# Performance work log

Measured on AMD Instinct MI355X. Metric: run time of the kernel, lower is better.

The kernel has to match this reference:

```python
import jax, jax.numpy as jnp
from jax import lax
import numpy as np

# ---- model dims ----
VOCAB, DMODEL, NLAYER = 32000, 1024, 4
NHEAD, HEAD = 16, 64              # RWKV6 heads (DMODEL = NHEAD*HEAD)
DIN = 2 * DMODEL                  # mamba expand=2
MHEAD, MHD = DIN // 64, 64        # mamba heads / head_dim (hard-coded 64 in block)
DSTATE, KCONV = 64, 4             # mamba2 state size / depthwise conv kernel
FFH = 4 * DMODEL
B, T = 1, 1024
EPS = 1e-6


def rmsnorm(v, w):
    return w * v * lax.rsqrt(jnp.mean(v * v, axis=-1, keepdims=True) + EPS)


def causal_dwconv(x, w):
    # x: [B,T,C], w: [C,K] depthwise causal conv
    C, K = w.shape
    xp = jnp.pad(x, ((0, 0), (K - 1, 0), (0, 0)))
    return lax.conv_general_dilated(
        xp, w.T[:, None, :], (1,), 'VALID',
        dimension_numbers=('NWC', 'WIO', 'NWC'), feature_group_count=C)


def setup_inputs() -> dict:
    key = jax.random.key(0)
    ks = iter(jax.random.split(key, 64))
    nrm = lambda shape, s=0.02: jax.random.normal(next(ks), shape, jnp.float32) * s
    x = jax.random.randint(next(ks), (B, T), 0, VOCAB)
    inp = dict(
        x=x,
        embed=nrm((VOCAB, DMODEL)),
        ln_w=jnp.ones((NLAYER, DMODEL), jnp.float32),
        Wr=nrm((NLAYER, DMODEL, DMODEL)), Wk=nrm((NLAYER, DMODEL, DMODEL)),
        Wv=nrm((NLAYER, DMODEL, DMODEL)), Ww=nrm((NLAYER, DMODEL, DMODEL)),
        w_bias=nrm((NLAYER, DMODEL), 0.5), u=nrm((NLAYER, NHEAD, HEAD), 0.5),
        Wg=nrm((NLAYER, DMODEL, DMODEL)), Wo=nrm((NLAYER, DMODEL, DMODEL)),
        Win=nrm((NLAYER, DMODEL, 2 * DIN + 2 * DSTATE + MHEAD)),
        conv_w=nrm((NLAYER, DIN + 2 * DSTATE, KCONV), 0.2),
        dt_bias=nrm((NLAYER, MHEAD), 0.5), A_log=nrm((NLAYER, MHEAD), 0.5),
        Dskip=nrm((NLAYER, MHEAD), 0.5),
        mnorm_w=jnp.ones((NLAYER, DIN), jnp.float32),
        Wout_m=nrm((NLAYER, DIN, DMODEL)),
        gate_w=nrm((NLAYER, 2 * DMODEL)), gate_b=jnp.zeros((NLAYER,), jnp.float32),
        ffn_ln_w=jnp.ones((NLAYER, DMODEL), jnp.float32),
        W1=nrm((NLAYER, DMODEL, FFH)), W2=nrm((NLAYER, FFH, DMODEL)),
        ln_out_w=jnp.ones((DMODEL,), jnp.float32),
    )
    return inp


def _block(h, p):
    (p_ln, pWr, pWk, pWv, pWw, p_wb, p_u, pWg, pWo, pWin, p_cw, p_dtb,
     p_Al, p_D, p_mn, pWom, p_gw, p_gb, p_fln, pW1, pW2) = p
    nx = rmsnorm(h, p_ln)

    # ---- RWKV6 linear attention ----
    r = (nx @ pWr).reshape(B, T, NHEAD, HEAD)
    k = (nx @ pWk).reshape(B, T, NHEAD, HEAD)
    v = (nx @ pWv).reshape(B, T, NHEAD, HEAD)
    dec = jnp.exp(-jnp.exp(nx @ pWw + p_wb)).reshape(B, T, NHEAD, HEAD)  # data-dep decay in (0,1)
    g = jax.nn.silu(nx @ pWg)

    def rstep(S, inp):
        rt, kt, vt, dt_ = inp                      # [B,H,hd]
        kv = kt[..., None] * vt[..., None, :]      # [B,H,hd,hd]
        o = jnp.einsum('bhk,bhkv->bhv', rt, S + p_u[None, :, :, None] * kv)
        return dt_[..., None] * S + kv, o

    S0 = jnp.zeros((B, NHEAD, HEAD, HEAD), nx.dtype)
    tmaj = lambda a: jnp.moveaxis(a, 1, 0)
    _, o = lax.scan(rstep, S0, (tmaj(r), tmaj(k), tmaj(v), tmaj(dec)))
    o = jnp.moveaxis(o, 0, 1).reshape(B, T, DMODEL)
    out_rwkv = (o * g) @ pWo

    # ---- Mamba2 selective scan ----
    zxbcdt = nx @ pWin
    z = zxbcdt[..., :DIN]
    xBC = zxbcdt[..., DIN:2 * DIN + 2 * DSTATE]
    dt = zxbcdt[..., -MHEAD:]
    xBC = jax.nn.silu(causal_dwconv(xBC, p_cw))
    xm = xBC[..., :DIN].reshape(B, T, MHEAD, MHD)
    Bm = xBC[..., DIN:DIN + DSTATE]
    Cm = xBC[..., DIN + DSTATE:]
    dt = jax.nn.softplus(dt + p_dtb)               # [B,T,MH]
    dA = jnp.exp(-dt * jnp.exp(p_Al))              # [B,T,MH]

    def mstep(hst, inp):
        xt, Bt, Ct, dAt, dtt = inp                 # [B,MH,hd],[B,ds],[B,ds],[B,MH],[B,MH]
        hst = dAt[..., None, None] * hst + (dtt[..., None] * xt)[..., None] * Bt[:, None, None, :]
        y = jnp.einsum('bhps,bs->bhp', hst, Ct)
        return hst, y

    h0 = jnp.zeros((B, MHEAD, MHD, DSTATE), nx.dtype)
    _, ym = lax.scan(mstep, h0, (tmaj(xm), tmaj(Bm), tmaj(Cm), tmaj(dA), tmaj(dt)))
    ym = jnp.moveaxis(ym, 0, 1) + p_D[None, None, :, None] * xm
    ym = ym.reshape(B, T, DIN)
    ym = rmsnorm(ym * jax.nn.silu(z), p_mn)        # gated RMSNorm
    out_mamba = ym @ pWom

    # ---- gated fusion + residual + FFN ----
    cat = jnp.concatenate([out_rwkv, out_mamba], axis=-1)
    gate = jax.nn.sigmoid(jnp.einsum('btd,d->bt', cat, p_gw) + p_gb)[..., None]
    h = h + gate * out_rwkv + (1.0 - gate) * out_mamba
    h = h + jax.nn.gelu(rmsnorm(h, p_fln) @ pW1, approximate=False) @ pW2
    return h


def reference(x, embed, ln_w, Wr, Wk, Wv, Ww, w_bias, u, Wg, Wo, Win, conv_w,
              dt_bias, A_log, Dskip, mnorm_w, Wout_m, gate_w, gate_b,
              ffn_ln_w, W1, W2, ln_out_w):
    h = embed[x]  # [B,T,D]
    params = (ln_w, Wr, Wk, Wv, Ww, w_bias, u, Wg, Wo, Win, conv_w, dt_bias,
              A_log, Dskip, mnorm_w, Wout_m, gate_w, gate_b, ffn_ln_w, W1, W2)
    h, _ = lax.scan(lambda c, p: (_block(c, p), None), h, params)
    logits = rmsnorm(h, ln_out_w) @ embed.T  # tied head
    return logits
```

## Files before the change

### kernel.cpp

```cpp
#include <hip/hip_runtime.h>
#include <hip/hip_bf16.h>
#include <math.h>

#define T 1024
#define NLAYER 4
#define NHEAD 16
#define HEAD 64
#define DIN 2048
#define MHEAD 32
#define DSTATE 64
#define FFH 4096
#define NWIN 4256
#define CCONV 2176
#define VOCABSZ 32000
#define NCHUNK 16
#define PKROWS 9472
#define PKN 9376

typedef unsigned short u16;
typedef __attribute__((ext_vector_type(8))) short s16x8;
typedef __attribute__((ext_vector_type(4))) float f32x4;

__device__ inline u16 f2bf(float f) {
  union { float f; unsigned u; } v; v.f = f;
  return (u16)((v.u + 0x7FFF + ((v.u >> 16) & 1)) >> 16);
}
__device__ inline float bf2f(u16 s) {
  union { unsigned u; float f; } v; v.u = ((unsigned)s) << 16;
  return v.f;
}
__device__ inline float sigf(float x) { return 1.f / (1.f + expf(-x)); }

__device__ inline void gload16(const void* g, void* l) {
  __builtin_amdgcn_global_load_lds(
      (__attribute__((address_space(1))) void*)(size_t)g,
      (__attribute__((address_space(3))) void*)(unsigned int)(size_t)l,
      16, 0, 0);
}

#define SWZ_SRC(lane) ((((lane) & 7) ^ ((lane) >> 3)) * 8)
#define SWZ_RD(kb, lk8, rsw) (((((kb) + (lk8)) >> 3) ^ (rsw)) << 3)

__device__ inline float block_sum(float v, float* sb) {
  #pragma unroll
  for (int o = 32; o; o >>= 1) v += __shfl_down(v, o);
  int w = threadIdx.x >> 6;
  if ((threadIdx.x & 63) == 0) sb[w] = v;
  __syncthreads();
  float s = sb[0] + sb[1] + sb[2] + sb[3];
  __syncthreads();
  return s;
}

__global__ __launch_bounds__(256) void k_cast(const float* __restrict__ s, u16* __restrict__ d) {
  size_t i = ((size_t)blockIdx.x * 256 + threadIdx.x) * 4;
  float4 v = *(const float4*)&s[i];
  u16 o[4] = {f2bf(v.x), f2bf(v.y), f2bf(v.z), f2bf(v.w)};
  *(uint2*)&d[i] = *(uint2*)o;
}

__global__ __launch_bounds__(256) void k_tcast(const float* __restrict__ src, size_t sstride,
                                               u16* __restrict__ dst, size_t dstride,
                                               int K, int N) {
  __shared__ float S[64][65];
  const float* sp = src + (size_t)blockIdx.z * sstride;
  u16* dp = dst + (size_t)blockIdx.z * dstride;
  int n0 = blockIdx.x * 64, k0 = blockIdx.y * 64;
  int tid = threadIdx.x;
  int tr = tid >> 4, tc = (tid & 15) * 4;
  #pragma unroll
  for (int it = 0; it < 4; ++it) {
    int r = tr + it * 16;
    int col = n0 + tc;
    float4 v;
    if (col + 3 < N) v = *(const float4*)&sp[(size_t)(k0 + r) * N + col];
    else {
      v.x = (col + 0 < N) ? sp[(size_t)(k0 + r) * N + col + 0] : 0.f;
      v.y = (col + 1 < N) ? sp[(size_t)(k0 + r) * N + col + 1] : 0.f;
      v.z = (col + 2 < N) ? sp[(size_t)(k0 + r) * N + col + 2] : 0.f;
      v.w = 0.f;
    }
    S[r][tc + 0] = v.x; S[r][tc + 1] = v.y; S[r][tc + 2] = v.z; S[r][tc + 3] = v.w;
  }
  __syncthreads();
  #pragma unroll
  for (int it = 0; it < 4; ++it) {
    int rn = tr + it * 16;
    if (n0 + rn >= N) continue;
    u16 o[4];
    o[0] = f2bf(S[tc + 0][rn]); o[1] = f2bf(S[tc + 1][rn]);
    o[2] = f2bf(S[tc + 2][rn]); o[3] = f2bf(S[tc + 3][rn]);
    *(uint2*)&dp[(size_t)(n0 + rn) * K + k0 + tc] = *(uint2*)o;
  }
}

struct TC6 { const float* src[6]; u16* dst[6]; size_t dstride[6]; };
__global__ __launch_bounds__(256) void k_tcast6(TC6 tc) {
  __shared__ float S[64][65];
  int w = blockIdx.z >> 2, l = blockIdx.z & 3;
  const float* sp = tc.src[w] + (size_t)l * 1024 * 1024;
  u16* dp = tc.dst[w] + (size_t)l * tc.dstride[w];
  int n0 = blockIdx.x * 64, k0 = blockIdx.y * 64;
  int tid = threadIdx.x;
  int tr = tid >> 4, tcc = (tid & 15) * 4;
  #pragma unroll
  for (int it = 0; it < 4; ++it) {
    int r = tr + it * 16;
    float4 v = *(const float4*)&sp[(size_t)(k0 + r) * 1024 + n0 + tcc];
    S[r][tcc + 0] = v.x; S[r][tcc + 1] = v.y; S[r][tcc + 2] = v.z; S[r][tcc + 3] = v.w;
  }
  __syncthreads();
  #pragma unroll
  for (int it = 0; it < 4; ++it) {
    int rn = tr + it * 16;
    u16 o[4];
    o[0] = f2bf(S[tcc + 0][rn]); o[1] = f2bf(S[tcc + 1][rn]);
    o[2] = f2bf(S[tcc + 2][rn]); o[3] = f2bf(S[tcc + 3][rn]);
    *(uint2*)&dp[(size_t)(n0 + rn) * 1024 + k0 + tcc] = *(uint2*)o;
  }
}

__global__ __launch_bounds__(256) void k_embln(const int* x, const float* embed,
                                               const float* w, float* h, u16* out) {
  __shared__ float sb[8];
  int t = blockIdx.x, tid = threadIdx.x;
  int row = x[t];
  float4 v = *(const float4*)&embed[(size_t)row * 1024 + tid * 4];
  *(float4*)&h[(size_t)t * 1024 + tid * 4] = v;
  float ss = v.x * v.x + v.y * v.y + v.z * v.z + v.w * v.w;
  float tot = block_sum(ss, sb);
  float rn = rsqrtf(tot / 1024.f + 1e-6f);
  int c = tid * 4;
  u16 o[4] = {f2bf(v.x * rn * w[c + 0]), f2bf(v.y * rn * w[c + 1]),
              f2bf(v.z * rn * w[c + 2]), f2bf(v.w * rn * w[c + 3])};
  *(uint2*)&out[(size_t)t * 1024 + c] = *(uint2*)o;
}

enum { EPI_F32 = 0, EPI_QKV = 1, EPI_GELU = 2 };

struct GOut {
  void* out;
  const float* aux;
  size_t zstride;
  float *r, *k, *v, *ld, *g, *zx;
};

template <int EPI, int BM, int BN>
__global__ __launch_bounds__(256) void k_gemm2(const u16* __restrict__ A,
                                               const u16* __restrict__ Bt,
                                               int N, int K, int kLen, GOut go) {
  __shared__ __align__(16) u16 smem[2][BM + BN][64];
  constexpr int FR = BM / 32, FC = BN / 32;
  constexpr int LPS = BM / 32 + BN / 32;
  int tid = threadIdx.x, lane = tid & 63, wid = tid >> 6;
  int lid = blockIdx.y * gridDim.x + blockIdx.x;
  int nwg = gridDim.x * gridDim.y;
  int q = nwg >> 3, r8 = nwg & 7;
  int xcd = lid & 7, pos = lid >> 3;
  int wg = (xcd < r8) ? (xcd * (q + 1) + pos) : (r8 * (q + 1) + (xcd - r8) * q + pos);
  int m0 = (wg % gridDim.x) * BM, n0 = (wg / gridDim.x) * BN;
  int kOff = blockIdx.z * kLen;
  int wr = (wid >> 1) * (BM / 2), wc = (wid & 1) * (BN / 2);
  int lr = lane & 15, lk8 = (lane >> 4) * 8;
  int rsw = lr & 7;
  int swc = SWZ_SRC(lane);
  int rA = lane >> 3;
  f32x4 acc[FR][FC] = {};

  auto STAGE = [&](int buf, int k0) {
    #pragma unroll
    for (int it = 0; it < BM / 32; ++it) {
      int rb = wid * (BM / 4) + it * 8;
      gload16(&A[(size_t)(m0 + rb + rA) * K + k0 + swc], &smem[buf][rb][0]);
    }
    #pragma unroll
    for (int it = 0; it < BN / 32; ++it) {
      int rb = wid * (BN / 4) + it * 8;
      gload16(&Bt[(size_t)(n0 + rb + rA) * K + k0 + swc], &smem[buf][BM + rb][0]);
    }
  };
  auto COMPUTE = [&](int buf) {
    #pragma unroll
    for (int kb = 0; kb < 64; kb += 32) {
      s16x8 af[FR], bf[FC];
      #pragma unroll
      for (int i = 0; i < FR; ++i)
        af[i] = *(const s16x8*)&smem[buf][wr + i * 16 + lr][SWZ_RD(kb, lk8, rsw)];
      #pragma unroll
      for (int j = 0; j < FC; ++j)
        bf[j] = *(const s16x8*)&smem[buf][BM + wc + j * 16 + lr][SWZ_RD(kb, lk8, rsw)];
      #pragma unroll
      for (int i = 0; i < FR; ++i)
        #pragma unroll
        for (int j = 0; j < FC; ++j)
          acc[i][j] = __builtin_amdgcn_mfma_f32_16x16x32_bf16(af[i], bf[j], acc[i][j], 0, 0, 0);
    }
  };

  int nt = kLen >> 6;
  STAGE(0, kOff);
  int cur = 0;
  for (int t = 0; t < nt; ++t) {
    if (t + 1 < nt) {
      STAGE(cur ^ 1, kOff + (t + 1) * 64);
      asm volatile("s_waitcnt vmcnt(%0)" :: "n"(LPS) : "memory");
    } else {
      asm volatile("s_waitcnt vmcnt(0)" ::: "memory");
    }
    __builtin_amdgcn_s_barrier();
    __builtin_amdgcn_sched_barrier(0);
    COMPUTE(cur);
    __builtin_amdgcn_s_barrier();
    cur ^= 1;
  }

  __syncthreads();
  float* cbuf = (float*)&smem[0][0][0];
  #pragma unroll
  for (int i = 0; i < FR; ++i)
    #pragma unroll
    for (int j = 0; j < FC; ++j) {
      int rrow = wr + i * 16 + ((lane >> 4) << 2);
      int ccol = wc + j * 16 + lr;
      #pragma unroll
      for (int r_ = 0; r_ < 4; ++r_)
        cbuf[(rrow + r_) * BN + ccol] = acc[i][j][r_];
    }
  __syncthreads();
  constexpr int RPB = BN / 4;
  constexpr int ITERS = (BM * RPB) / 256;
  if constexpr (EPI == EPI_F32) {
    float* outf = (float*)go.out + (size_t)blockIdx.z * go.zstride;
    #pragma unroll
    for (int it2 = 0; it2 < ITERS; ++it2) {
      int idx = it2 * 256 + tid;
      int row = idx / RPB, c4 = (idx % RPB) * 4;
      int gc = n0 + c4;
      if (gc >= N) continue;
      float4 v = *(const float4*)&cbuf[row * BN + c4];
      if (gc + 3 < N) *(float4*)&outf[(size_t)(m0 + row) * N + gc] = v;
      else {
        const float* pv = (const float*)&v;
        for (int e = 0; e < 4 && gc + e < N; ++e)
          outf[(size_t)(m0 + row) * N + gc + e] = pv[e];
      }
    }
  } else if constexpr (EPI == EPI_GELU) {
    u16* outb = (u16*)go.out;
    #pragma unroll
    for (int it2 = 0; it2 < ITERS; ++it2) {
      int idx = it2 * 256 + tid;
      int row = idx / RPB, c4 = (idx % RPB) * 4;
      int gc = n0 + c4;
      if (gc + 3 >= N) continue;
      float4 v = *(const float4*)&cbuf[row * BN + c4];
      u16 o[4];
      o[0] = f2bf(0.5f * v.x * (1.f + erff(v.x * 0.70710678118654752f)));
      o[1] = f2bf(0.5f * v.y * (1.f + erff(v.y * 0.70710678118654752f)));
      o[2] = f2bf(0.5f * v.z * (1.f + erff(v.z * 0.70710678118654752f)));
      o[3] = f2bf(0.5f * v.w * (1.f + erff(v.w * 0.70710678118654752f)));
      *(uint2*)&outb[(size_t)(m0 + row) * N + gc] = *(uint2*)o;
    }
  } else {
    float* tptr; int ldbw, coff, op;
    if (n0 < 5120) {
      int tsel = n0 >> 10;
      tptr = (tsel == 0) ? go.r : (tsel == 1) ? go.k : (tsel == 2) ? go.v
           : (tsel == 3) ? go.ld : go.g;
      ldbw = 1024; coff = n0 & 1023;
      op = (tsel == 3) ? 1 : (tsel == 4) ? 2 : 0;
    } else {
      tptr = go.zx; ldbw = 4256; coff = n0 - 5120; op = 0;
    }
    #pragma unroll
    for (int it2 = 0; it2 < ITERS; ++it2) {
      int idx = it2 * 256 + tid;
      int row = idx / RPB, c4 = (idx % RPB) * 4;
      int gc = n0 + c4;
      if (gc >= N) continue;
      float4 v = *(const float4*)&cbuf[row * BN + c4];
      float* pv = (float*)&v;
      if (op == 1) {
        #pragma unroll
        for (int e = 0; e < 4; ++e) pv[e] = -expf(pv[e] + go.aux[coff + c4 + e]);
      } else if (op == 2) {
        #pragma unroll
        for (int e = 0; e < 4; ++e) pv[e] = pv[e] * sigf(pv[e]);
      }
      if (gc + 3 < N) *(float4*)&tptr[(size_t)(m0 + row) * ldbw + coff + c4] = v;
      else {
        for (int e = 0; e < 4 && gc + e < N; ++e)
          tptr[(size_t)(m0 + row) * ldbw + coff + c4 + e] = pv[e];
      }
    }
  }
}

struct DualArg {
  const u16 *A0, *A1, *B0, *B1;
  float *o0, *o1;
  int K0, K1;
};
__global__ __launch_bounds__(256) void k_dual(DualArg da) {
  __shared__ __align__(16) u16 smem[2][128][64];
  const u16* A  = blockIdx.z ? da.A1 : da.A0;
  const u16* Bt = blockIdx.z ? da.B1 : da.B0;
  float* out    = blockIdx.z ? da.o1 : da.o0;
  int K         = blockIdx.z ? da.K1 : da.K0;
  const int N = 1024;
  int tid = threadIdx.x, lane = tid & 63, wid = tid >> 6;
  int lid = blockIdx.y * gridDim.x + blockIdx.x;
  int nwg = gridDim.x * gridDim.y;
  int q = nwg >> 3, r8 = nwg & 7;
  int xcd = lid & 7, pos = lid >> 3;
  int wg = (xcd < r8) ? (xcd * (q + 1) + pos) : (r8 * (q + 1) + (xcd - r8) * q + pos);
  int m0 = (wg % gridDim.x) * 64, n0 = (wg / gridDim.x) * 64;
  int wr = (wid >> 1) * 32, wc = (wid & 1) * 32;
  int lr = lane & 15, lk8 = (lane >> 4) * 8;
  int rsw = lr & 7, swc = SWZ_SRC(lane), rA = lane >> 3;
  f32x4 acc[2][2] = {};
  auto STAGE = [&](int buf, int k0) {
    #pragma unroll
    for (int it = 0; it < 2; ++it) {
      int rb = wid * 16 + it * 8;
      gload16(&A[(size_t)(m0 + rb + rA) * K + k0 + swc], &smem[buf][rb][0]);
      gload16(&Bt[(size_t)(n0 + rb + rA) * K + k0 + swc], &smem[buf][64 + rb][0]);
    }
  };
  auto COMPUTE = [&](int buf) {
    #pragma unroll
    for (int kb = 0; kb < 64; kb += 32) {
      s16x8 af[2], bf[2];
      #pragma unroll
      for (int i = 0; i < 2; ++i)
        af[i] = *(const s16x8*)&smem[buf][wr + i * 16 + lr][SWZ_RD(kb, lk8, rsw)];
      #pragma unroll
      for (int j = 0; j < 2; ++j)
        bf[j] = *(const s16x8*)&smem[buf][64 + wc + j * 16 + lr][SWZ_RD(kb, lk8, rsw)];
      #pragma unroll
      for (int i = 0; i < 2; ++i)
        #pragma unroll
        for (int j = 0; j < 2; ++j)
          acc[i][j] = __builtin_amdgcn_mfma_f32_16x16x32_bf16(af[i], bf[j], acc[i][j], 0, 0, 0);
    }
  };
  int nt = K >> 6;
  STAGE(0, 0);
  int cur = 0;
  for (int t = 0; t < nt; ++t) {
    if (t + 1 < nt) {
      STAGE(cur ^ 1, (t + 1) * 64);
      asm volatile("s_waitcnt vmcnt(4)" ::: "memory");
    } else {
      asm volatile("s_waitcnt vmcnt(0)" ::: "memory");
    }
    __builtin_amdgcn_s_barrier();
    __builtin_amdgcn_sched_barrier(0);
    COMPUTE(cur);
    __builtin_amdgcn_s_barrier();
    cur ^= 1;
  }
  __syncthreads();
  float* cbuf = (float*)&smem[0][0][0];
  #pragma unroll
  for (int i = 0; i < 2; ++i)
    #pragma unroll
    for (int j = 0; j < 2; ++j) {
      int rrow = wr + i * 16 + ((lane >> 4) << 2);
      int ccol = wc + j * 16 + lr;
      #pragma unroll
      for (int r_ = 0; r_ < 4; ++r_)
        cbuf[(rrow + r_) * 64 + ccol] = acc[i][j][r_];
    }
  __syncthreads();
  #pragma unroll
  for (int it2 = 0; it2 < 4; ++it2) {
    int idx = it2 * 256 + tid;
    int row = idx >> 4, c4 = (idx & 15) * 4;
    *(float4*)&out[(size_t)(m0 + row) * N + n0 + c4] = *(const float4*)&cbuf[row * 64 + c4];
  }
}

__global__ __launch_bounds__(256) void k_conv(const float* __restrict__ zx,
                                              const float* __restrict__ cw,
                                              float* __restrict__ xc) {
  int c = (blockIdx.x * 256 + threadIdx.x) * 4;
  int t = blockIdx.y;
  if (c >= CCONV) return;
  float4 w0 = *(const float4*)&cw[(c + 0) * 4];
  float4 w1 = *(const float4*)&cw[(c + 1) * 4];
  float4 w2 = *(const float4*)&cw[(c + 2) * 4];
  float4 w3 = *(const float4*)&cw[(c + 3) * 4];
  float4 a = {0.f, 0.f, 0.f, 0.f};
  #pragma unroll
  for (int tap = 0; tap < 4; ++tap) {
    int tt = t - 3 + tap;
    if (tt < 0) continue;
    float4 z = *(const float4*)&zx[(size_t)tt * NWIN + 2048 + c];
    a.x += z.x * ((const float*)&w0)[tap];
    a.y += z.y * ((const float*)&w1)[tap];
    a.z += z.z * ((const float*)&w2)[tap];
    a.w += z.w * ((const float*)&w3)[tap];
  }
  a.x = a.x * sigf(a.x); a.y = a.y * sigf(a.y);
  a.z = a.z * sigf(a.z); a.w = a.w * sigf(a.w);
  *(float4*)&xc[(size_t)t * CCONV + c] = a;
}

__global__ __launch_bounds__(256) void k_dtbc(const float* __restrict__ zx,
                                              const float* __restrict__ xc,
                                              const float* __restrict__ dt_bias,
                                              const float* __restrict__ A_log,
                                              float* __restrict__ dtb, float* __restrict__ la,
                                              float* __restrict__ BC) {
  int c = blockIdx.x, tid = threadIdx.x;
  if (blockIdx.y == 0) {
    __shared__ float ldaS[64][33];
    #pragma unroll
    for (int it = 0; it < 8; ++it) {
      int e = it * 256 + tid;
      int i = e >> 5, j = e & 31;
      float x = zx[(size_t)(c * 64 + i) * NWIN + 4224 + j] + dt_bias[j];
      float sp = (x > 20.f) ? x : log1pf(expf(x));
      dtb[(size_t)(c * 64 + i) * 32 + j] = sp;
      ldaS[i][j] = -sp * expf(A_log[j]);
    }
    __syncthreads();
    if (tid < 32) {
      float g = 0.f;
      for (int i = 0; i < 64; ++i) {
        g += ldaS[i][tid];
        la[((size_t)c * 32 + tid) * 64 + i] = g;
      }
    }
  } else {
    __shared__ float Bc[64][65];
    __shared__ float Cc[16][65];
    int i0 = (blockIdx.y - 1) * 16;
    #pragma unroll
    for (int it = 0; it < 4; ++it) {
      int idx = it * 256 + tid;
      int r = idx >> 4, c4 = (idx & 15) * 4;
      float4 b4 = *(const float4*)&xc[(size_t)(c * 64 + r) * CCONV + 2048 + c4];
      Bc[r][c4] = b4.x; Bc[r][c4+1] = b4.y; Bc[r][c4+2] = b4.z; Bc[r][c4+3] = b4.w;
    }
    {
      int r = tid >> 4, c4 = (tid & 15) * 4;
      float4 cv = *(const float4*)&xc[(size_t)(c * 64 + i0 + r) * CCONV + 2112 + c4];
      Cc[r][c4] = cv.x; Cc[r][c4+1] = cv.y; Cc[r][c4+2] = cv.z; Cc[r][c4+3] = cv.w;
    }
    __syncthreads();
    int il = tid >> 4, sg = tid & 15;
    float acc[4] = {};
    for (int d = 0; d < 64; ++d) {
      float cv = Cc[il][d];
      #pragma unroll
      for (int j = 0; j < 4; ++j) acc[j] += Bc[sg * 4 + j][d] * cv;
    }
    #pragma unroll
    for (int j = 0; j < 4; ++j)
      BC[((size_t)c * 64 + i0 + il) * 64 + sg * 4 + j] = acc[j];
  }
}

union SmemH1 {
  struct { float rS[64][66], kS[64][66], gS[64][66]; u16 khS[64][64]; u16 vtS[64][72]; float uS[64]; } a;
  struct { u16 XT[64][72], BT[64][72]; float fS[64]; } b;
};
__global__ __launch_bounds__(256) void k_heads1(const float* __restrict__ rbuf,
                                                const float* __restrict__ kbuf,
                                                const float* __restrict__ ldbuf,
                                                const float* __restrict__ vbuf,
                                                const float* __restrict__ u,
                                                const float* __restrict__ xc,
                                                const float* __restrict__ la,
                                                const float* __restrict__ dtb,
                                                u16* __restrict__ rt, float* __restrict__ eL,
                                                u16* __restrict__ G, float* __restrict__ U,
                                                float* __restrict__ Um) {
  __shared__ SmemH1 sm;
  int c = blockIdx.x, tid = threadIdx.x;
  int lane = tid & 63, wid = tid >> 6;
  int lr = lane & 15, lk8 = (lane >> 4) * 8, rsw = lr & 7;
  int wr = (wid >> 1) * 32, wc = (wid & 1) * 32;
  if (blockIdx.y < 16) {
    int h = blockIdx.y;
    #pragma unroll
    for (int it = 0; it < 4; ++it) {
      int idx = it * 256 + tid;
      int i = idx >> 4, c4 = (idx & 15) * 4;
      size_t base = (size_t)(c * 64 + i) * 1024 + h * 64 + c4;
      float4 rv = *(const float4*)&rbuf[base];
      float4 kv = *(const float4*)&kbuf[base];
      float4 lv = *(const float4*)&ldbuf[base];
      float4 vv = *(const float4*)&vbuf[base];
      sm.a.rS[i][c4] = rv.x; sm.a.rS[i][c4+1] = rv.y; sm.a.rS[i][c4+2] = rv.z; sm.a.rS[i][c4+3] = rv.w;
      sm.a.kS[i][c4] = kv.x; sm.a.kS[i][c4+1] = kv.y; sm.a.kS[i][c4+2] = kv.z; sm.a.kS[i][c4+3] = kv.w;
      sm.a.gS[i][c4] = lv.x; sm.a.gS[i][c4+1] = lv.y; sm.a.gS[i][c4+2] = lv.z; sm.a.gS[i][c4+3] = lv.w;
      sm.a.vtS[c4 + 0][i] = f2bf(vv.x); sm.a.vtS[c4 + 1][i] = f2bf(vv.y);
      sm.a.vtS[c4 + 2][i] = f2bf(vv.z); sm.a.vtS[c4 + 3][i] = f2bf(vv.w);
    }
    if (tid < 64) sm.a.uS[tid] = u[h * 64 + tid];
    __syncthreads();
    if (tid < 64) {
      int k = tid;
      float g = 0.f;
      for (int i = 0; i < 64; ++i) {
        float ld = sm.a.gS[i][k];
        sm.a.gS[i][k] = g;
        rt[(size_t)(c * 64 + i) * 1024 + h * 64 + k] = f2bf(sm.a.rS[i][k] * __expf(g));
        g += ld;
      }
      float gL = g;
      eL[((size_t)c * 16 + h) * 64 + k] = __expf(gL);
      for (int i = 0; i < 64; ++i) {
        float gincl = (i < 63) ? sm.a.gS[i + 1][k] : gL;
        int col = (((i >> 3) ^ (k & 7)) << 3) | (i & 7);
        sm.a.khS[k][col] = f2bf(sm.a.kS[i][k] * __expf(fminf(gL - gincl, 0.f)));
      }
    }
    __syncthreads();
    {
      int i = tid & 63, sg = tid >> 6;
      float acc[16] = {};
      float accd = 0.f;
      for (int k = 0; k < 64; ++k) {
        float rv = sm.a.rS[i][k], gi = sm.a.gS[i][k];
        accd += rv * sm.a.uS[k] * sm.a.kS[i][k];
        #pragma unroll
        for (int j = 0; j < 16; ++j) {
          int s = sg * 16 + j;
          int sp1 = (s < 63) ? s + 1 : 63;
          acc[j] += rv * sm.a.kS[s][k] * __expf(fminf(gi - sm.a.gS[sp1][k], 0.f));
        }
      }
      #pragma unroll
      for (int j = 0; j < 16; ++j) {
        int s = sg * 16 + j;
        float v = (s < i) ? acc[j] : ((s == i) ? accd : 0.f);
        G[(((size_t)c * 16 + h) * 64 + i) * 64 + s] = f2bf(v);
      }
    }
    {
      size_t gb = ((size_t)c * 16 + h) * 64;
      f32x4 acc2[2][2] = {};
      #pragma unroll
      for (int kb = 0; kb < 64; kb += 32) {
        s16x8 a[2], b[2];
        #pragma unroll
        for (int i_ = 0; i_ < 2; ++i_)
          a[i_] = *(const s16x8*)&sm.a.khS[wr + i_ * 16 + lr][SWZ_RD(kb, lk8, rsw)];
        #pragma unroll
        for (int j_ = 0; j_ < 2; ++j_)
          b[j_] = *(const s16x8*)&sm.a.vtS[wc + j_ * 16 + lr][kb + lk8];
        #pragma unroll
        for (int i_ = 0; i_ < 2; ++i_)
          #pragma unroll
          for (int j_ = 0; j_ < 2; ++j_)
            acc2[i_][j_] = __builtin_amdgcn_mfma_f32_16x16x32_bf16(a[i_], b[j_], acc2[i_][j_], 0, 0, 0);
      }
      #pragma unroll
      for (int i_ = 0; i_ < 2; ++i_)
        #pragma unroll
        for (int j_ = 0; j_ < 2; ++j_) {
          int row = wr + i_ * 16 + ((lane >> 4) << 2);
          int col = wc + j_ * 16 + lr;
          #pragma unroll
          for (int r_ = 0; r_ < 4; ++r_)
            U[(gb + row + r_) * 64 + col] = acc2[i_][j_][r_];
        }
    }
  } else {
    int h = blockIdx.y - 16;
    size_t lb = ((size_t)c * 32 + h) * 64;
    if (tid < 64) {
      float la63 = la[lb + 63];
      sm.b.fS[tid] = dtb[(size_t)(c * 64 + tid) * 32 + h] * __expf(fminf(la63 - la[lb + tid], 0.f));
    }
    __syncthreads();
    #pragma unroll
    for (int it = 0; it < 4; ++it) {
      int idx = it * 256 + tid;
      int t = idx >> 4, p4 = (idx & 15) * 4;
      float f = sm.b.fS[t];
      float4 xv = *(const float4*)&xc[(size_t)(c * 64 + t) * CCONV + h * 64 + p4];
      sm.b.XT[p4 + 0][t] = f2bf(f * xv.x); sm.b.XT[p4 + 1][t] = f2bf(f * xv.y);
      sm.b.XT[p4 + 2][t] = f2bf(f * xv.z); sm.b.XT[p4 + 3][t] = f2bf(f * xv.w);
      float4 bv = *(const float4*)&xc[(size_t)(c * 64 + t) * CCONV + 2048 + p4];
      sm.b.BT[p4 + 0][t] = f2bf(bv.x); sm.b.BT[p4 + 1][t] = f2bf(bv.y);
      sm.b.BT[p4 + 2][t] = f2bf(bv.z); sm.b.BT[p4 + 3][t] = f2bf(bv.w);
    }
    __syncthreads();
    f32x4 acc[2][2] = {};
    #pragma unroll
    for (int kb = 0; kb < 64; kb += 32) {
      s16x8 a[2], b[2];
      #pragma unroll
      for (int i = 0; i < 2; ++i) a[i] = *(const s16x8*)&sm.b.XT[wr + i * 16 + lr][kb + lk8];
      #pragma unroll
      for (int j = 0; j < 2; ++j) b[j] = *(const s16x8*)&sm.b.BT[wc + j * 16 + lr][kb + lk8];
      #pragma unroll
      for (int i = 0; i < 2; ++i)
        #pragma unroll
        for (int j = 0; j < 2; ++j)
          acc[i][j] = __builtin_amdgcn_mfma_f32_16x16x32_bf16(a[i], b[j], acc[i][j], 0, 0, 0);
    }
    #pragma unroll
    for (int i = 0; i < 2; ++i)
      #pragma unroll
      for (int j = 0; j < 2; ++j) {
        int row = wr + i * 16 + ((lane >> 4) << 2);
        int col = wc + j * 16 + lr;
        #pragma unroll
        for (int r_ = 0; r_ < 4; ++r_)
          Um[(lb + row + r_) * 64 + col] = acc[i][j][r_];
      }
  }
}

__global__ __launch_bounds__(256) void k_scan2(const float* __restrict__ Urw,
                                               const float* __restrict__ eL,
                                               u16* __restrict__ Sall,
                                               const float* __restrict__ Um,
                                               const float* __restrict__ la,
                                               u16* __restrict__ hall) {
  int tid = threadIdx.x;
  if (blockIdx.x < 16) {
    int h = blockIdx.x;
    int k = tid >> 2, v0 = blockIdx.y * 16 + (tid & 3) * 4;
    float S[4] = {};
    for (int c = 0; c < 16; ++c) {
      size_t gb = ((size_t)c * 16 + h) * 64;
      u16 tmp[4] = {f2bf(S[0]), f2bf(S[1]), f2bf(S[2]), f2bf(S[3])};
      *(uint2*)&Sall[(gb + k) * 64 + v0] = *(uint2*)&tmp[0];
      float e = eL[gb + k];
      float4 uv = *(const float4*)&Urw[(gb + k) * 64 + v0];
      S[0] = e * S[0] + uv.x; S[1] = e * S[1] + uv.y;
      S[2] = e * S[2] + uv.z; S[3] = e * S[3] + uv.w;
    }
  } else {
    int h = blockIdx.x - 16;
    int p = tid >> 2, s0 = blockIdx.y * 16 + (tid & 3) * 4;
    float S[4] = {};
    for (int c = 0; c < 16; ++c) {
      size_t lb = ((size_t)c * 32 + h) * 64;
      u16 tmp[4] = {f2bf(S[0]), f2bf(S[1]), f2bf(S[2]), f2bf(S[3])};
      *(uint2*)&hall[(lb + p) * 64 + s0] = *(uint2*)&tmp[0];
      float e = __expf(la[lb + 63]);
      float4 uv = *(const float4*)&Um[(lb + p) * 64 + s0];
      S[0] = e * S[0] + uv.x; S[1] = e * S[1] + uv.y;
      S[2] = e * S[2] + uv.z; S[3] = e * S[3] + uv.w;
    }
  }
}

union SmemH2 {
  struct { u16 rtS[64][64], GS[64][64], StS[64][72], vtS[64][72]; } a;
  struct { u16 MS[64][64], hS[64][64], CtS[64][72], XT2[64][72]; float laS[64], dtbS[64], eS[64]; } b;
};
__global__ __launch_bounds__(256) void k_heads2(const u16* __restrict__ rt,
                                                const u16* __restrict__ Gb,
                                                const u16* __restrict__ Sall,
                                                const float* __restrict__ vbuf,
                                                const float* __restrict__ gbuf,
                                                u16* __restrict__ og,
                                                const u16* __restrict__ hall,
                                                const float* __restrict__ xc,
                                                const float* __restrict__ la,
                                                const float* __restrict__ dtb,
                                                const float* __restrict__ BC,
                                                float* __restrict__ ymb) {
  __shared__ SmemH2 sm;
  int c = blockIdx.x, tid = threadIdx.x;
  int lane = tid & 63, wid = tid >> 6;
  int lr = lane & 15, lk8 = (lane >> 4) * 8;
  int rsw = lr & 7, swc = SWZ_SRC(lane);
  int wr = (wid >> 1) * 32, wc = (wid & 1) * 32;
  if (blockIdx.y < 16) {
    int h = blockIdx.y;
    size_t gb = ((size_t)c * 16 + h) * 64;
    #pragma unroll
    for (int it = 0; it < 2; ++it) {
      int rb = wid * 16 + it * 8;
      int r = rb + (lane >> 3);
      gload16(&rt[(size_t)(c * 64 + r) * 1024 + h * 64 + swc], &sm.a.rtS[rb][0]);
      gload16(&Gb[(gb + r) * 64 + swc], &sm.a.GS[rb][0]);
    }
    #pragma unroll
    for (int it = 0; it < 2; ++it) {
      int idx = it * 256 + tid;
      int k = idx >> 3, c8 = (idx & 7) * 8;
      uint4 ld = *(const uint4*)&Sall[(gb + k) * 64 + c8];
      const u16* pv = (const u16*)&ld;
      #pragma unroll
      for (int jj = 0; jj < 8; ++jj) sm.a.StS[c8 + jj][k] = pv[jj];
    }
    #pragma unroll
    for (int it = 0; it < 4; ++it) {
      int idx = it * 256 + tid;
      int s = idx >> 4, v4 = (idx & 15) * 4;
      float4 vv = *(const float4*)&vbuf[(size_t)(c * 64 + s) * 1024 + h * 64 + v4];
      sm.a.vtS[v4 + 0][s] = f2bf(vv.x); sm.a.vtS[v4 + 1][s] = f2bf(vv.y);
      sm.a.vtS[v4 + 2][s] = f2bf(vv.z); sm.a.vtS[v4 + 3][s] = f2bf(vv.w);
    }
    __syncthreads();
    f32x4 acc[2][2] = {};
    #pragma unroll
    for (int kb = 0; kb < 64; kb += 32) {
      s16x8 aR[2], aG[2], bS[2], bV[2];
      #pragma unroll
      for (int i = 0; i < 2; ++i) {
        aR[i] = *(const s16x8*)&sm.a.rtS[wr + i * 16 + lr][SWZ_RD(kb, lk8, rsw)];
        aG[i] = *(const s16x8*)&sm.a.GS[wr + i * 16 + lr][SWZ_RD(kb, lk8, rsw)];
      }
      #pragma unroll
      for (int j = 0; j < 2; ++j) {
        bS[j] = *(const s16x8*)&sm.a.StS[wc + j * 16 + lr][kb + lk8];
        bV[j] = *(const s16x8*)&sm.a.vtS[wc + j * 16 + lr][kb + lk8];
      }
      #pragma unroll
      for (int i = 0; i < 2; ++i)
        #pragma unroll
        for (int j = 0; j < 2; ++j) {
          acc[i][j] = __builtin_amdgcn_mfma_f32_16x16x32_bf16(aR[i], bS[j], acc[i][j], 0, 0, 0);
          acc[i][j] = __builtin_amdgcn_mfma_f32_16x16x32_bf16(aG[i], bV[j], acc[i][j], 0, 0, 0);
        }
    }
    #pragma unroll
    for (int i = 0; i < 2; ++i)
      #pragma unroll
      for (int j = 0; j < 2; ++j) {
        int row = c * 64 + wr + i * 16 + ((lane >> 4) << 2);
        int col = h * 64 + wc + j * 16 + lr;
        #pragma unroll
        for (int r_ = 0; r_ < 4; ++r_) {
          size_t idx = (size_t)(row + r_) * 1024 + col;
          og[idx] = f2bf(acc[i][j][r_] * gbuf[idx]);
        }
      }
  } else {
    int h = blockIdx.y - 16;
    size_t lb = ((size_t)c * 32 + h) * 64;
    if (tid < 64) {
      float lv = la[lb + tid];
      sm.b.laS[tid] = lv;
      sm.b.eS[tid] = __expf(lv);
      sm.b.dtbS[tid] = dtb[(size_t)(c * 64 + tid) * 32 + h];
    }
    #pragma unroll
    for (int it = 0; it < 2; ++it) {
      int rb = wid * 16 + it * 8;
      int r = rb + (lane >> 3);
      gload16(&hall[(lb + r) * 64 + swc], &sm.b.hS[rb][0]);
    }
    __syncthreads();
    #pragma unroll
    for (int it = 0; it < 4; ++it) {
      int idx = it * 256 + tid;
      int i = idx >> 4, s4 = (idx & 15) * 4;
      float lai = sm.b.laS[i];
      float4 bc4 = *(const float4*)&BC[((size_t)c * 64 + i) * 64 + s4];
      u16 mo[4];
      #pragma unroll
      for (int j = 0; j < 4; ++j) {
        int s = s4 + j;
        float bcv = (j == 0) ? bc4.x : (j == 1) ? bc4.y : (j == 2) ? bc4.z : bc4.w;
        float v = 0.f;
        if (s <= i)
          v = __expf(fminf(lai - sm.b.laS[s], 0.f)) * sm.b.dtbS[s] * bcv;
        mo[j] = f2bf(v);
      }
      *(uint2*)&sm.b.MS[i][(((s4 >> 3) ^ (i & 7)) << 3) | (s4 & 7)] = *(uint2*)mo;
      float ei = sm.b.eS[i];
      float4 cv = *(const float4*)&xc[(size_t)(c * 64 + i) * CCONV + 2112 + s4];
      sm.b.CtS[i][s4 + 0] = f2bf(ei * cv.x); sm.b.CtS[i][s4 + 1] = f2bf(ei * cv.y);
      sm.b.CtS[i][s4 + 2] = f2bf(ei * cv.z); sm.b.CtS[i][s4 + 3] = f2bf(ei * cv.w);
      float4 xv = *(const float4*)&xc[(size_t)(c * 64 + i) * CCONV + h * 64 + s4];
      sm.b.XT2[s4 + 0][i] = f2bf(xv.x); sm.b.XT2[s4 + 1][i] = f2bf(xv.y);
      sm.b.XT2[s4 + 2][i] = f2bf(xv.z); sm.b.XT2[s4 + 3][i] = f2bf(xv.w);
    }
    __syncthreads();
    f32x4 acc[2][2] = {};
    #pragma unroll
    for (int kb = 0; kb < 64; kb += 32) {
      s16x8 aM[2], aC[2], bX[2], bH[2];
      #pragma unroll
      for (int i = 0; i < 2; ++i) {
        aM[i] = *(const s16x8*)&sm.b.MS[wr + i * 16 + lr][SWZ_RD(kb, lk8, rsw)];
        aC[i] = *(const s16x8*)&sm.b.CtS[wr + i * 16 + lr][kb + lk8];
      }
      #pragma unroll
      for (int j = 0; j < 2; ++j) {
        bX[j] = *(const s16x8*)&sm.b.XT2[wc + j * 16 + lr][kb + lk8];
        bH[j] = *(const s16x8*)&sm.b.hS[wc + j * 16 + lr][SWZ_RD(kb, lk8, rsw)];
      }
      #pragma unroll
      for (int i = 0; i < 2; ++i)
        #pragma unroll
        for (int j = 0; j < 2; ++j) {
          acc[i][j] = __builtin_amdgcn_mfma_f32_16x16x32_bf16(aM[i], bX[j], acc[i][j], 0, 0, 0);
          acc[i][j] = __builtin_amdgcn_mfma_f32_16x16x32_bf16(aC[i], bH[j], acc[i][j], 0, 0, 0);
        }
    }
    #pragma unroll
    for (int i = 0; i < 2; ++i)
      #pragma unroll
      for (int j = 0; j < 2; ++j) {
        int row = c * 64 + wr + i * 16 + ((lane >> 4) << 2);
        int col = h * 64 + wc + j * 16 + lr;
        #pragma unroll
        for (int r_ = 0; r_ < 4; ++r_)
          ymb[(size_t)(row + r_) * 2048 + col] = acc[i][j][r_];
      }
  }
}

__global__ __launch_bounds__(256) void k_ymn(const float* ymb, const float* xc,
                                             const float* zx, const float* Dsk,
                                             const float* mnw, u16* out) {
  __shared__ float sb[8];
  int t = blockIdx.x, tid = threadIdx.x;
  float vals[8];
  float ss = 0.f;
  #pragma unroll
  for (int j = 0; j < 8; ++j) {
    int cidx = j * 256 + tid;
    float yv = ymb[(size_t)t * 2048 + cidx] + Dsk[cidx >> 6] * xc[(size_t)t * CCONV + cidx];
    float zv = zx[(size_t)t * NWIN + cidx];
    float val = yv * zv * sigf(zv);
    vals[j] = val;
    ss += val * val;
  }
  float tot = block_sum(ss, sb);
  float rn = rsqrtf(tot / 2048.f + 1e-6f);
  #pragma unroll
  for (int j = 0; j < 8; ++j) {
    int cidx = j * 256 + tid;
    out[(size_t)t * 2048 + cidx] = f2bf(vals[j] * rn * mnw[cidx]);
  }
}

__global__ __launch_bounds__(256) void k_gateln(const float* rw, const float* mb,
                                                const float* gw, const float* gb,
                                                float* h, const float* w, u16* nx) {
  __shared__ float sb[8];
  int t = blockIdx.x, tid = threadIdx.x;
  float s = 0.f;
  #pragma unroll
  for (int j = 0; j < 4; ++j) {
    int d = j * 256 + tid;
    s += rw[(size_t)t * 1024 + d] * gw[d] + mb[(size_t)t * 1024 + d] * gw[1024 + d];
  }
  float tot = block_sum(s, sb);
  float gate = sigf(tot + gb[0]);
  float hv[4], ss = 0.f;
  #pragma unroll
  for (int j = 0; j < 4; ++j) {
    int d = j * 256 + tid;
    float v = h[(size_t)t * 1024 + d] + gate * rw[(size_t)t * 1024 + d] +
              (1.f - gate) * mb[(size_t)t * 1024 + d];
    h[(size_t)t * 1024 + d] = v;
    hv[j] = v;
    ss += v * v;
  }
  float tot2 = block_sum(ss, sb);
  float rn = rsqrtf(tot2 / 1024.f + 1e-6f);
  #pragma unroll
  for (int j = 0; j < 4; ++j) {
    int d = j * 256 + tid;
    nx[(size_t)t * 1024 + d] = f2bf(hv[j] * rn * w[d]);
  }
}

__global__ __launch_bounds__(256) void k_redln(const float* __restrict__ part,
                                               float* __restrict__ h,
                                               const float* __restrict__ w,
                                               u16* __restrict__ nx) {
  __shared__ float sb[8];
  int t = blockIdx.x, tid = threadIdx.x;
  size_t base = (size_t)t * 1024 + tid * 4;
  float4 s = *(const float4*)&part[base];
  #pragma unroll
  for (int p = 1; p < 4; ++p) {
    float4 v = *(const float4*)&part[(size_t)p * 1024 * 1024 + base];
    s.x += v.x; s.y += v.y; s.z += v.z; s.w += v.w;
  }
  float4 d = *(const float4*)&h[base];
  s.x += d.x; s.y += d.y; s.z += d.z; s.w += d.w;
  *(float4*)&h[base] = s;
  float ss = s.x * s.x + s.y * s.y + s.z * s.z + s.w * s.w;
  float tot = block_sum(ss, sb);
  float rn = rsqrtf(tot / 1024.f + 1e-6f);
  int c = tid * 4;
  u16 o[4] = {f2bf(s.x * rn * w[c + 0]), f2bf(s.y * rn * w[c + 1]),
              f2bf(s.z * rn * w[c + 2]), f2bf(s.w * rn * w[c + 3])};
  *(uint2*)&nx[(size_t)t * 1024 + c] = *(uint2*)o;
}

extern "C" void kernel_launch(void* const* d_in, const int* in_sizes, int n_in,
                              void* d_out, int out_size, void* d_ws, size_t ws_size,
                              hipStream_t stream) {
  const int*   x       = (const int*)d_in[0];
  const float* embed   = (const float*)d_in[1];
  const float* ln_w    = (const float*)d_in[2];
  const float* Wr      = (const float*)d_in[3];
  const float* Wk      = (const float*)d_in[4];
  const float* Wv      = (const float*)d_in[5];
  const float* Ww      = (const float*)d_in[6];
  const float* w_bias  = (const float*)d_in[7];
  const float* u       = (const float*)d_in[8];
  const float* Wg      = (const float*)d_in[9];
  const float* Wo      = (const float*)d_in[10];
  const float* Win     = (const float*)d_in[11];
  const float* conv_w  = (const float*)d_in[12];
  const float* dt_bias = (const float*)d_in[13];
  const float* A_log   = (const float*)d_in[14];
  const float* Dskip   = (const float*)d_in[15];
  const float* mnorm_w = (const float*)d_in[16];
  const float* Wout_m  = (const float*)d_in[17];
  const float* gate_w  = (const float*)d_in[18];
  const float* gate_b  = (const float*)d_in[19];
  const float* ffn_ln  = (const float*)d_in[20];
  const float* W1      = (const float*)d_in[21];
  const float* W2      = (const float*)d_in[22];
  const float* ln_out  = (const float*)d_in[23];

  char* p = (char*)d_ws;
  auto alloc = [&](size_t bytes) {
    char* r = p;
    p += (bytes + 255) & ~(size_t)255;
    return r;
  };
  u16* embB = (u16*)alloc((size_t)VOCABSZ * 1024 * 2);
  u16* Wpk  = (u16*)alloc((size_t)NLAYER * PKROWS * 1024 * 2);
  u16* WoT  = (u16*)alloc((size_t)NLAYER * 1024 * 1024 * 2);
  u16* WomT = (u16*)alloc((size_t)NLAYER * 1024 * 2048 * 2);
  u16* W1T  = (u16*)alloc((size_t)NLAYER * 4096 * 1024 * 2);
  u16* W2T  = (u16*)alloc((size_t)NLAYER * 1024 * 4096 * 2);
  float* h        = (float*)alloc((size_t)T * 1024 * 4);
  u16*   nx       = (u16*)alloc((size_t)T * 1024 * 2);
  float* rbuf     = (float*)alloc((size_t)T * 1024 * 4);
  float* kbuf     = (float*)alloc((size_t)T * 1024 * 4);
  float* vbuf     = (float*)alloc((size_t)T * 1024 * 4);
  float* ldbuf    = (float*)alloc((size_t)T * 1024 * 4);
  float* gbuf     = (float*)alloc((size_t)T * 1024 * 4);
  float* zx       = (float*)alloc((size_t)T * NWIN * 4);
  u16*   rt       = (u16*)alloc((size_t)T * 1024 * 2);
  float* eL       = (float*)alloc((size_t)NCHUNK * 16 * 64 * 4);
  u16*   Gb       = (u16*)alloc((size_t)NCHUNK * 16 * 64 * 64 * 2);
  float* Urw      = (float*)alloc((size_t)NCHUNK * 16 * 64 * 64 * 4);
  u16*   Sall     = (u16*)alloc((size_t)NCHUNK * 16 * 64 * 64 * 2);
  u16*   og       = (u16*)alloc((size_t)T * 1024 * 2);
  float* out_rwkv = (float*)alloc((size_t)T * 1024 * 4);
  float* xc       = (float*)alloc((size_t)T * CCONV * 4);
  float* dtb      = (float*)alloc((size_t)T * 32 * 4);
  float* la       = (float*)alloc((size_t)NCHUNK * 32 * 64 * 4);
  float* BC       = (float*)alloc((size_t)NCHUNK * 64 * 64 * 4);
  float* Um       = (float*)alloc((size_t)NCHUNK * 32 * 64 * 64 * 4);
  u16*   hall     = (u16*)alloc((size_t)NCHUNK * 32 * 64 * 64 * 2);
  float* ymb      = (float*)alloc((size_t)T * 2048 * 4);
  u16*   ymn      = (u16*)alloc((size_t)T * 2048 * 2);
  float* out_mam  = (float*)alloc((size_t)T * 1024 * 4);
  u16*   ffa      = (u16*)alloc((size_t)T * FFH * 2);
  float* part     = (float*)alloc((size_t)4 * 1024 * 1024 * 4);

  const size_t PKS = (size_t)PKROWS * 1024;

  k_cast<<<VOCABSZ * 1024 / 1024, 256, 0, stream>>>(embed, embB);
  {
    TC6 tc;
    tc.src[0] = Wr; tc.src[1] = Wk; tc.src[2] = Wv; tc.src[3] = Ww; tc.src[4] = Wg; tc.src[5] = Wo;
    tc.dst[0] = Wpk;               tc.dstride[0] = PKS;
    tc.dst[1] = Wpk + 1024 * 1024; tc.dstride[1] = PKS;
    tc.dst[2] = Wpk + 2048 * 1024; tc.dstride[2] = PKS;
    tc.dst[3] = Wpk + 3072 * 1024; tc.dstride[3] = PKS;
    tc.dst[4] = Wpk + 4096 * 1024; tc.dstride[4] = PKS;
    tc.dst[5] = WoT;               tc.dstride[5] = (size_t)1024 * 1024;
    k_tcast6<<<dim3(16, 16, 24), 256, 0, stream>>>(tc);
  }
  k_tcast<<<dim3(67, 16, 4), 256, 0, stream>>>(Win, (size_t)1024 * NWIN, Wpk + (size_t)5120 * 1024, PKS, 1024, NWIN);
  k_tcast<<<dim3(16, 32, 4), 256, 0, stream>>>(Wout_m, (size_t)2048 * 1024, WomT, (size_t)1024 * 2048, 2048, 1024);
  k_tcast<<<dim3(64, 16, 4), 256, 0, stream>>>(W1, (size_t)1024 * 4096, W1T, (size_t)4096 * 1024, 1024, 4096);
  k_tcast<<<dim3(16, 64, 4), 256, 0, stream>>>(W2, (size_t)4096 * 1024, W2T, (size_t)1024 * 4096, 4096, 1024);

  k_embln<<<1024, 256, 0, stream>>>(x, embed, ln_w, h, nx);

  for (int l = 0; l < NLAYER; ++l) {
    {
      GOut go = {};
      go.r = rbuf; go.k = kbuf; go.v = vbuf; go.ld = ldbuf; go.g = gbuf; go.zx = zx;
      go.aux = w_bias + l * 1024;
      k_gemm2<EPI_QKV, 128, 128><<<dim3(8, 74), 256, 0, stream>>>(nx, Wpk + (size_t)l * PKS, PKN, 1024, 1024, go);
    }
    k_conv<<<dim3(3, 1024), 256, 0, stream>>>(zx, conv_w + (size_t)l * CCONV * 4, xc);
    k_dtbc<<<dim3(16, 5), 256, 0, stream>>>(zx, xc, dt_bias + l * 32, A_log + l * 32, dtb, la, BC);
    k_heads1<<<dim3(16, 48), 256, 0, stream>>>(rbuf, kbuf, ldbuf, vbuf, u + (size_t)l * 1024,
                                               xc, la, dtb, rt, eL, Gb, Urw, Um);
    k_scan2<<<dim3(48, 4), 256, 0, stream>>>(Urw, eL, Sall, Um, la, hall);
    k_heads2<<<dim3(16, 48), 256, 0, stream>>>(rt, Gb, Sall, vbuf, gbuf, og,
                                               hall, xc, la, dtb, BC, ymb);
    k_ymn<<<1024, 256, 0, stream>>>(ymb, xc, zx, Dskip + l * 32, mnorm_w + (size_t)l * 2048, ymn);
    {
      DualArg da;
      da.A0 = og;  da.B0 = WoT + (size_t)l * 1024 * 1024;  da.o0 = out_rwkv; da.K0 = 1024;
      da.A1 = ymn; da.B1 = WomT + (size_t)l * 1024 * 2048; da.o1 = out_mam;  da.K1 = 2048;
      k_dual<<<dim3(16, 16, 2), 256, 0, stream>>>(da);
    }
    k_gateln<<<1024, 256, 0, stream>>>(out_rwkv, out_mam, gate_w + (size_t)l * 2048,
                                       gate_b + l, h, ffn_ln + l * 1024, nx);
    {
      GOut go = {}; go.out = ffa;
      k_gemm2<EPI_GELU, 128, 128><<<dim3(8, 32), 256, 0, stream>>>(nx, W1T + (size_t)l * 4096 * 1024, 4096, 1024, 1024, go);
    }
    {
      GOut go = {}; go.out = part; go.zstride = (size_t)1024 * 1024;
      k_gemm2<EPI_F32, 64, 64><<<dim3(16, 16, 4), 256, 0, stream>>>(ffa, W2T + (size_t)l * 1024 * 4096, 1024, 4096, 1024, go);
    }
    k_redln<<<1024, 256, 0, stream>>>(part, h,
                                      (l < NLAYER - 1) ? (ln_w + (l + 1) * 1024) : ln_out, nx);
  }

  {
    GOut go = {}; go.out = d_out;
    k_gemm2<EPI_F32, 128, 128><<<dim3(8, 250), 256, 0, stream>>>(nx, embB, VOCABSZ, 1024, 1024, go);
  }
}
```

Baseline: 1.106 ms.

## Generalize GEMM to 512-thread blocks and store F32 outputs directly from registers

The GEMM kernel is templated on thread count, so 128x128 tiles now run with 8 waves in a 4x2 layout instead of 4 waves, which halves the accumulator fragments per wave and adds latency hiding. Staging loads are unified across the A and B rows. The F32 epilogue now writes accumulators straight to global memory, dropping the LDS round-trip and two barriers, but the stores become scalar and strided per lane instead of float4 rows. The larger blocks may also lower how many workgroups fit per CU.

```diff
diff --git a/kernel.cpp b/kernel.cpp
--- a/kernel.cpp
+++ b/kernel.cpp
@@ -145,13 +145,18 @@
   float *r, *k, *v, *ld, *g, *zx;
 };
 
-template <int EPI, int BM, int BN>
-__global__ __launch_bounds__(256) void k_gemm2(const u16* __restrict__ A,
-                                               const u16* __restrict__ Bt,
-                                               int N, int K, int kLen, GOut go) {
+template <int EPI, int BM, int BN, int TH>
+__global__ __launch_bounds__(TH) void k_gemm2(const u16* __restrict__ A,
+                                              const u16* __restrict__ Bt,
+                                              int N, int K, int kLen, GOut go) {
   __shared__ __align__(16) u16 smem[2][BM + BN][64];
-  constexpr int FR = BM / 32, FC = BN / 32;
-  constexpr int LPS = BM / 32 + BN / 32;
+  constexpr int NW = TH / 64;
+  constexpr int NWM = (NW == 8) ? 4 : 2;
+  constexpr int NWN = NW / NWM;
+  constexpr int FR = BM / NWM / 16, FC = BN / NWN / 16;
+  constexpr int ROWS = BM + BN;
+  constexpr int RPW = ROWS / NW;
+  constexpr int LPS = RPW / 8;
   int tid = threadIdx.x, lane = tid & 63, wid = tid >> 6;
   int lid = blockIdx.y * gridDim.x + blockIdx.x;
   int nwg = gridDim.x * gridDim.y;
@@ -160,7 +165,7 @@
   int wg = (xcd < r8) ? (xcd * (q + 1) + pos) : (r8 * (q + 1) + (xcd - r8) * q + pos);
   int m0 = (wg % gridDim.x) * BM, n0 = (wg / gridDim.x) * BN;
   int kOff = blockIdx.z * kLen;
-  int wr = (wid >> 1) * (BM / 2), wc = (wid & 1) * (BN / 2);
+  int wr = (wid / NWN) * (BM / NWM), wc = (wid % NWN) * (BN / NWN);
   int lr = lane & 15, lk8 = (lane >> 4) * 8;
   int rsw = lr & 7;
   int swc = SWZ_SRC(lane);
@@ -169,14 +174,12 @@
 
   auto STAGE = [&](int buf, int k0) {
     #pragma unroll
-    for (int it = 0; it < BM / 32; ++it) {
-      int rb = wid * (BM / 4) + it * 8;
-      gload16(&A[(size_t)(m0 + rb + rA) * K + k0 + swc], &smem[buf][rb][0]);
-    }
-    #pragma unroll
-    for (int it = 0; it < BN / 32; ++it) {
-      int rb = wid * (BN / 4) + it * 8;
-      gload16(&Bt[(size_t)(n0 + rb + rA) * K + k0 + swc], &smem[buf][BM + rb][0]);
+    for (int it = 0; it < LPS; ++it) {
+      int rb = wid * RPW + it * 8;
+      if (rb < BM)
+        gload16(&A[(size_t)(m0 + rb + rA) * K + k0 + swc], &smem[buf][rb][0]);
+      else
+        gload16(&Bt[(size_t)(n0 + rb - BM + rA) * K + k0 + swc], &smem[buf][rb][0]);
     }
   };
   auto COMPUTE = [&](int buf) {
@@ -214,83 +217,82 @@
     cur ^= 1;
   }
 
-  __syncthreads();
-  float* cbuf = (float*)&smem[0][0][0];
-  #pragma unroll
-  for (int i = 0; i < FR; ++i)
-    #pragma unroll
-    for (int j = 0; j < FC; ++j) {
-      int rrow = wr + i * 16 + ((lane >> 4) << 2);
-      int ccol = wc + j * 16 + lr;
-      #pragma unroll
-      for (int r_ = 0; r_ < 4; ++r_)
-        cbuf[(rrow + r_) * BN + ccol] = acc[i][j][r_];
-    }
-  __syncthreads();
-  constexpr int RPB = BN / 4;
-  constexpr int ITERS = (BM * RPB) / 256;
   if constexpr (EPI == EPI_F32) {
     float* outf = (float*)go.out + (size_t)blockIdx.z * go.zstride;
     #pragma unroll
-    for (int it2 = 0; it2 < ITERS; ++it2) {
-      int idx = it2 * 256 + tid;
-      int row = idx / RPB, c4 = (idx % RPB) * 4;
-      int gc = n0 + c4;
-      if (gc >= N) continue;
-      float4 v = *(const float4*)&cbuf[row * BN + c4];
-      if (gc + 3 < N) *(float4*)&outf[(size_t)(m0 + row) * N + gc] = v;
-      else {
-        const float* pv = (const float*)&v;
-        for (int e = 0; e < 4 && gc + e < N; ++e)
-          outf[(size_t)(m0 + row) * N + gc + e] = pv[e];
-      }
-    }
-  } else if constexpr (EPI == EPI_GELU) {
-    u16* outb = (u16*)go.out;
-    #pragma unroll
-    for (int it2 = 0; it2 < ITERS; ++it2) {
-      int idx = it2 * 256 + tid;
-      int row = idx / RPB, c4 = (idx % RPB) * 4;
-      int gc = n0 + c4;
-      if (gc + 3 >= N) continue;
-      float4 v = *(const float4*)&cbuf[row * BN + c4];
-      u16 o[4];
-      o[0] = f2bf(0.5f * v.x * (1.f + erff(v.x * 0.70710678118654752f)));
-      o[1] = f2bf(0.5f * v.y * (1.f + erff(v.y * 0.70710678118654752f)));
-      o[2] = f2bf(0.5f * v.z * (1.f + erff(v.z * 0.70710678118654752f)));
-      o[3] = f2bf(0.5f * v.w * (1.f + erff(v.w * 0.70710678118654752f)));
-      *(uint2*)&outb[(size_t)(m0 + row) * N + gc] = *(uint2*)o;
-    }
+    for (int i = 0; i < FR; ++i)
+      #pragma unroll
+      for (int j = 0; j < FC; ++j) {
+        int row = m0 + wr + i * 16 + ((lane >> 4) << 2);
+        int col = n0 + wc + j * 16 + lr;
+        if (col >= N) continue;
+        #pragma unroll
+        for (int r_ = 0; r_ < 4; ++r_)
+          outf[(size_t)(row + r_) * N + col] = acc[i][j][r_];
+      }
   } else {
-    float* tptr; int ldbw, coff, op;
-    if (n0 < 5120) {
-      int tsel = n0 >> 10;
-      tptr = (tsel == 0) ? go.r : (tsel == 1) ? go.k : (tsel == 2) ? go.v
-           : (tsel == 3) ? go.ld : go.g;
-      ldbw = 1024; coff = n0 & 1023;
-      op = (tsel == 3) ? 1 : (tsel == 4) ? 2 : 0;
+    __syncthreads();
+    float* cbuf = (float*)&smem[0][0][0];
+    #pragma unroll
+    for (int i = 0; i < FR; ++i)
+      #pragma unroll
+      for (int j = 0; j < FC; ++j) {
+        int rrow = wr + i * 16 + ((lane >> 4) << 2);
+        int ccol = wc + j * 16 + lr;
+        #pragma unroll
+        for (int r_ = 0; r_ < 4; ++r_)
+          cbuf[(rrow + r_) * BN + ccol] = acc[i][j][r_];
+      }
+    __syncthreads();
+    constexpr int RPB = BN / 4;
+    constexpr int ITERS = (BM * RPB) / TH;
+    if constexpr (EPI == EPI_GELU) {
+      u16* outb = (u16*)go.out;
+      #pragma unroll
+      for (int it2 = 0; it2 < ITERS; ++it2) {
+        int idx = it2 * TH + tid;
+        int row = idx / RPB, c4 = (idx % RPB) * 4;
+        int gc = n0 + c4;
+        if (gc + 3 >= N) continue;
+        float4 v = *(const float4*)&cbuf[row * BN + c4];
+        u16 o[4];
+        o[0] = f2bf(0.5f * v.x * (1.f + erff(v.x * 0.70710678118654752f)));
+        o[1] = f2bf(0.5f * v.y * (1.f + erff(v.y * 0.70710678118654752f)));
+        o[2] = f2bf(0.5f * v.z * (1.f + erff(v.z * 0.70710678118654752f)));
+        o[3] = f2bf(0.5f * v.w * (1.f + erff(v.w * 0.70710678118654752f)));
+        *(uint2*)&outb[(size_t)(m0 + row) * N + gc] = *(uint2*)o;
+      }
     } else {
-      tptr = go.zx; ldbw = 4256; coff = n0 - 5120; op = 0;
-    }
-    #pragma unroll
-    for (int it2 = 0; it2 < ITERS; ++it2) {
-      int idx = it2 * 256 + tid;
-      int row = idx / RPB, c4 = (idx % RPB) * 4;
-      int gc = n0 + c4;
-      if (gc >= N) continue;
-      float4 v = *(const float4*)&cbuf[row * BN + c4];
-      float* pv = (float*)&v;
-      if (op == 1) {
-        #pragma unroll
-        for (int e = 0; e < 4; ++e) pv[e] = -expf(pv[e] + go.aux[coff + c4 + e]);
-      } else if (op == 2) {
-        #pragma unroll
-        for (int e = 0; e < 4; ++e) pv[e] = pv[e] * sigf(pv[e]);
-      }
-      if (gc + 3 < N) *(float4*)&tptr[(size_t)(m0 + row) * ldbw + coff + c4] = v;
-      else {
-        for (int e = 0; e < 4 && gc + e < N; ++e)
-          tptr[(size_t)(m0 + row) * ldbw + coff + c4 + e] = pv[e];
+      float* tptr; int ldbw, coff, op;
+      if (n0 < 5120) {
+        int tsel = n0 >> 10;
+        tptr = (tsel == 0) ? go.r : (tsel == 1) ? go.k : (tsel == 2) ? go.v
+             : (tsel == 3) ? go.ld : go.g;
+        ldbw = 1024; coff = n0 & 1023;
+        op = (tsel == 3) ? 1 : (tsel == 4) ? 2 : 0;
+      } else {
+        tptr = go.zx; ldbw = 4256; coff = n0 - 5120; op = 0;
+      }
+      #pragma unroll
+      for (int it2 = 0; it2 < ITERS; ++it2) {
+        int idx = it2 * TH + tid;
+        int row = idx / RPB, c4 = (idx % RPB) * 4;
+        int gc = n0 + c4;
+        if (gc >= N) continue;
+        float4 v = *(const float4*)&cbuf[row * BN + c4];
+        float* pv = (float*)&v;
+        if (op == 1) {
+          #pragma unroll
+          for (int e = 0; e < 4; ++e) pv[e] = -expf(pv[e] + go.aux[coff + c4 + e]);
+        } else if (op == 2) {
+          #pragma unroll
+          for (int e = 0; e < 4; ++e) pv[e] = pv[e] * sigf(pv[e]);
+        }
+        if (gc + 3 < N) *(float4*)&tptr[(size_t)(m0 + row) * ldbw + coff + c4] = v;
+        else {
+          for (int e = 0; e < 4 && gc + e < N; ++e)
+            tptr[(size_t)(m0 + row) * ldbw + coff + c4 + e] = pv[e];
+        }
       }
     }
   }
@@ -990,7 +992,7 @@
       GOut go = {};
       go.r = rbuf; go.k = kbuf; go.v = vbuf; go.ld = ldbuf; go.g = gbuf; go.zx = zx;
       go.aux = w_bias + l * 1024;
-      k_gemm2<EPI_QKV, 128, 128><<<dim3(8, 74), 256, 0, stream>>>(nx, Wpk + (size_t)l * PKS, PKN, 1024, 1024, go);
+      k_gemm2<EPI_QKV, 128, 128, 512><<<dim3(8, 74), 512, 0, stream>>>(nx, Wpk + (size_t)l * PKS, PKN, 1024, 1024, go);
     }
     k_conv<<<dim3(3, 1024), 256, 0, stream>>>(zx, conv_w + (size_t)l * CCONV * 4, xc);
     k_dtbc<<<dim3(16, 5), 256, 0, stream>>>(zx, xc, dt_bias + l * 32, A_log + l * 32, dtb, la, BC);
@@ -1010,11 +1012,11 @@
                                        gate_b + l, h, ffn_ln + l * 1024, nx);
     {
       GOut go = {}; go.out = ffa;
-      k_gemm2<EPI_GELU, 128, 128><<<dim3(8, 32), 256, 0, stream>>>(nx, W1T + (size_t)l * 4096 * 1024, 4096, 1024, 1024, go);
+      k_gemm2<EPI_GELU, 128, 128, 512><<<dim3(8, 32), 512, 0, stream>>>(nx, W1T + (size_t)l * 4096 * 1024, 4096, 1024, 1024, go);
     }
     {
       GOut go = {}; go.out = part; go.zstride = (size_t)1024 * 1024;
-      k_gemm2<EPI_F32, 64, 64><<<dim3(16, 16, 4), 256, 0, stream>>>(ffa, W2T + (size_t)l * 1024 * 4096, 1024, 4096, 1024, go);
+      k_gemm2<EPI_F32, 64, 64, 256><<<dim3(16, 16, 4), 256, 0, stream>>>(ffa, W2T + (size_t)l * 1024 * 4096, 1024, 4096, 1024, go);
     }
     k_redln<<<1024, 256, 0, stream>>>(part, h,
                                       (l < NLAYER - 1) ? (ln_w + (l + 1) * 1024) : ln_out, nx);
@@ -1022,6 +1024,6 @@
 
   {
     GOut go = {}; go.out = d_out;
-    k_gemm2<EPI_F32, 128, 128><<<dim3(8, 250), 256, 0, stream>>>(nx, embB, VOCABSZ, 1024, 1024, go);
-  }
-}
+    k_gemm2<EPI_F32, 128, 128, 512><<<dim3(8, 250), 512, 0, stream>>>(nx, embB, VOCABSZ, 1024, 1024, go);
+  }
+}
```

Measured after the change: 1.040 ms. 1.06x faster.
